# Performance work log

Measured on AMD Instinct MI355X. Metric: run time of the kernel, lower is better.

Reference implementation:

```python
import jax, jax.numpy as jnp
import numpy as np

N, P, E = 100000, 10000, 500000
DN, DP, DK, SKIP, MLP_H = 256, 128, 100, 27, 64
E_MEAN, E_STD = 4.0, 2.0
ETA_MEAN, ETA_STD = 0.0, 1.5
ATT_NORM = 0.1  # 1/sqrt(100)
LN_EPS, RMS_EPS = 1e-5, 1e-6


def setup_inputs() -> dict:
    key = jax.random.key(0)
    ks = jax.random.split(key, 32)
    DIN = DN + SKIP  # 283
    s = 0.05
    inp = {
        'node_hidden': jax.random.normal(ks[0], (N, DN), jnp.float32),
        'energy': jax.random.uniform(ks[1], (N,), jnp.float32, 0.01, 1.0),
        'eta': jax.random.normal(ks[2], (N,), jnp.float32),
        'phi': jax.random.normal(ks[3], (N,), jnp.float32),
        'layer': jax.random.uniform(ks[4], (N,), jnp.float32),
        'eta_l': jax.random.normal(ks[5], (N, 6), jnp.float32),
        'phi_l': jax.random.normal(ks[6], (N, 6), jnp.float32),
        'ene_l': jax.random.normal(ks[7], (N, 6), jnp.float32),
        'track_feats': jax.random.uniform(ks[8], (N, 5), jnp.float32),
        'particle_hidden': jax.random.normal(ks[9], (P, DP), jnp.float32),
        'global_rep': jax.random.normal(ks[10], (P, DN), jnp.float32),
        'edge_src': jax.random.randint(ks[11], (E,), 0, N, jnp.int32),
        'edge_dst': jax.random.randint(ks[12], (E,), 0, P, jnp.int32),
        # learned params
        'W_key': jax.random.normal(ks[13], (DIN, DK), jnp.float32) * s,
        'b_key': jnp.zeros((DK,), jnp.float32),
        'W_val': jax.random.normal(ks[14], (DIN, DP), jnp.float32) * s,
        'b_val': jnp.zeros((DP,), jnp.float32),
        'W_q': jax.random.normal(ks[15], (DP + DN, DK), jnp.float32) * s,
        'b_q': jnp.zeros((DK,), jnp.float32),
        'W_ih': jax.random.normal(ks[16], (DP, 3 * DP), jnp.float32) * s,
        'b_ih': jnp.zeros((3 * DP,), jnp.float32),
        'W_hh': jax.random.normal(ks[17], (DP, 3 * DP), jnp.float32) * s,
        'b_hh': jnp.zeros((3 * DP,), jnp.float32),
        'ln_g': jnp.ones((DP,), jnp.float32),
        'ln_b': jnp.zeros((DP,), jnp.float32),
        'W1': jax.random.normal(ks[18], (DP, MLP_H), jnp.float32) * s,
        'b1': jnp.zeros((MLP_H,), jnp.float32),
        'W2': jax.random.normal(ks[19], (MLP_H, DP), jnp.float32) * s,
        'b2': jnp.zeros((DP,), jnp.float32),
        'rms_w': jnp.ones((DP,), jnp.float32),
        'lin_w': jax.random.normal(ks[20], (1, DP), jnp.float32),
    }
    return inp


def _forward(node_hidden, energy, eta, phi, layer, eta_l, phi_l, ene_l, track_feats,
             particle_hidden, global_rep,
             W_key, b_key, W_val, b_val, W_q, b_q, W_ih, b_ih, W_hh, b_hh,
             ln_g, ln_b, W1, b1, W2, b2, rms_w, lin_w, edge_src, edge_dst):
    # --- build node inputs: hidden rep + 27 skip scalars (same order as torch cat) ---
    skip = jnp.concatenate([
        ((jnp.log(energy) - E_MEAN) / E_STD)[:, None],
        ((eta - ETA_MEAN) / ETA_STD)[:, None],
        phi[:, None], layer[:, None],
        (eta_l - ETA_MEAN) / ETA_STD,  # eta_l1..l6
        phi_l, ene_l,
        track_feats,  # isTrack, nTracks, tracks_pt, nTracks_4, tracks_pt_4
    ], axis=1)  # [N, 27]
    x = jnp.concatenate([node_hidden, skip], axis=1)  # [N, 283]
    keys = x @ W_key + b_key      # [N, 100]
    vals = x @ W_val + b_val      # [N, DP]
    q = jnp.concatenate([particle_hidden, global_rep], axis=1) @ W_q + b_q  # [P, 100]

    # --- per-edge attention (note: node_update consumes RAW relu attention) ---
    att = jax.nn.relu(jnp.sum(keys[edge_src] * q[edge_dst], axis=1) * ATT_NORM)  # [E]
    msg = att[:, None] * vals[edge_src]                                          # [E, DP]
    ws = jax.ops.segment_sum(msg, edge_dst, num_segments=P)                      # [P, DP]

    # --- node update: rmsnorm * sigmoid(eltwise) gating, GRU, LN, MLP residual ---
    rms = ws * jax.lax.rsqrt(jnp.mean(ws * ws, axis=-1, keepdims=True) + RMS_EPS) * rms_w
    gated = rms * jax.nn.sigmoid(ws * lin_w)

    h = particle_hidden
    gi = gated @ W_ih + b_ih
    gh = h @ W_hh + b_hh
    i_r, i_z, i_n = jnp.split(gi, 3, axis=1)
    h_r, h_z, h_n = jnp.split(gh, 3, axis=1)
    r = jax.nn.sigmoid(i_r + h_r)
    z = jax.nn.sigmoid(i_z + h_z)
    n = jnp.tanh(i_n + r * h_n)
    h_new = (1.0 - z) * n + z * h

    mu = jnp.mean(h_new, axis=-1, keepdims=True)
    var = jnp.mean((h_new - mu) ** 2, axis=-1, keepdims=True)
    ln = (h_new - mu) * jax.lax.rsqrt(var + LN_EPS) * ln_g + ln_b
    mlp = jax.nn.relu(ln @ W1 + b1) @ W2 + b2
    return h + mlp  # updated particle 'node hidden rep'


def reference(node_hidden, energy, eta, phi, layer, eta_l, phi_l, ene_l, track_feats,
              particle_hidden, global_rep, edge_src, edge_dst,
              W_key, b_key, W_val, b_val, W_q, b_q, W_ih, b_ih, W_hh, b_hh,
              ln_g, ln_b, W1, b1, W2, b2, rms_w, lin_w):
    return _forward(node_hidden, energy, eta, phi, layer, eta_l, phi_l, ene_l, track_feats,
                    particle_hidden, global_rep,
                    W_key, b_key, W_val, b_val, W_q, b_q, W_ih, b_ih, W_hh, b_hh,
                    ln_g, ln_b, W1, b1, W2, b2, rms_w, lin_w, edge_src, edge_dst)
```

## Files before the change

### kernel.cpp

```cpp
#include <hip/hip_runtime.h>
#include <hip/hip_bf16.h>
#include <math.h>

#define THREADS 256

typedef __bf16 bf16_t;
typedef __bf16 bf16x8 __attribute__((ext_vector_type(8)));
typedef float f32x4 __attribute__((ext_vector_type(4)));

__device__ __forceinline__ float sigmoidf_(float x) { return 1.f / (1.f + expf(-x)); }

__device__ __forceinline__ void gload_lds16(const void* g, void* l) {
    __builtin_amdgcn_global_load_lds((const __attribute__((address_space(1))) void*)g,
                                     (__attribute__((address_space(3))) void*)l, 16, 0, 0);
}

__global__ void prep_kernel(const float* __restrict__ W_key, const float* __restrict__ W_val,
                            const float* __restrict__ W_q, const float* __restrict__ b_key,
                            const float* __restrict__ b_val, const float* __restrict__ b_q,
                            bf16_t* __restrict__ WbfT, bf16_t* __restrict__ WqT,
                            float* __restrict__ bpn, float* __restrict__ bpq)
{
    int i = blockIdx.x * THREADS + threadIdx.x;
    const int NW = 256 * 288, NQ = 128 * 384;
    if (i < NW) {
        int c = i / 288, k = i - c * 288;
        float v = 0.f;
        if (k < 283) {
            if (c < 100) v = W_key[k * 100 + c];
            else if (c >= 128 && c < 256) v = W_val[k * 128 + (c - 128)];
        }
        WbfT[i] = (bf16_t)v;
    } else if (i < NW + NQ) {
        int j = i - NW;
        int c = j / 384, k = j - c * 384;
        WqT[j] = (bf16_t)((c < 100) ? W_q[k * 100 + c] : 0.f);
    } else if (i < NW + NQ + 256) {
        int c = i - NW - NQ;
        bpn[c] = (c < 100) ? b_key[c] : ((c >= 128 && c < 256) ? b_val[c - 128] : 0.f);
    } else if (i < NW + NQ + 256 + 128) {
        int c = i - NW - NQ - 256;
        bpq[c] = (c < 100) ? b_q[c] : 0.f;
    }
}

__global__ void prep2_kernel(const float* __restrict__ W_ih, const float* __restrict__ W_hh,
                             const float* __restrict__ b_ih, const float* __restrict__ b_hh,
                             const float* __restrict__ W1, const float* __restrict__ b1,
                             const float* __restrict__ W2,
                             bf16_t* __restrict__ BTg, bf16_t* __restrict__ W1Tp,
                             bf16_t* __restrict__ W2Tp, float* __restrict__ bgru,
                             float* __restrict__ b1p)
{
    int i = blockIdx.x * THREADS + threadIdx.x;
    const int NG = 768 * 256, N1 = 128 * 128, N2 = 128 * 128;
    if (i < NG) {
        int c = i >> 8, k = i & 255;
        float v = 0.f;
        if (c < 384) { if (k < 128) v = W_ih[k * 384 + c]; }
        else         { if (k >= 128) v = W_hh[(k - 128) * 384 + (c - 384)]; }
        BTg[i] = (bf16_t)v;
    } else if (i < NG + N1) {
        int j = i - NG; int c = j >> 7, k = j & 127;
        W1Tp[j] = (bf16_t)((c < 64) ? W1[k * 64 + c] : 0.f);
    } else if (i < NG + N1 + N2) {
        int j = i - NG - N1; int c = j >> 7, k = j & 127;
        W2Tp[j] = (bf16_t)((k < 64) ? W2[k * 128 + c] : 0.f);
    } else if (i < NG + N1 + N2 + 768) {
        int c = i - NG - N1 - N2;
        bgru[c] = (c < 384) ? b_ih[c] : b_hh[c - 384];
    } else if (i < NG + N1 + N2 + 768 + 128) {
        int c = i - NG - N1 - N2 - 768;
        b1p[c] = (c < 64) ? b1[c] : 0.f;
    }
}

__global__ void convertA_kernel(const float* __restrict__ nh, bf16_t* __restrict__ Abf, int N_)
{
    int id = blockIdx.x * THREADS + threadIdx.x;
    int row = id >> 5, cc = id & 31;
    bf16x8 v = {};
    if (row < N_) {
        const float* p = nh + (size_t)row * 256 + cc * 8;
        float4 a = *(const float4*)p;
        float4 b = *(const float4*)(p + 4);
        v[0] = (bf16_t)a.x; v[1] = (bf16_t)a.y; v[2] = (bf16_t)a.z; v[3] = (bf16_t)a.w;
        v[4] = (bf16_t)b.x; v[5] = (bf16_t)b.y; v[6] = (bf16_t)b.z; v[7] = (bf16_t)b.w;
    }
    *(bf16x8*)(Abf + (size_t)row * 288 + cc * 8) = v;
}

__global__ void skip_kernel(const float* __restrict__ energy, const float* __restrict__ eta,
                            const float* __restrict__ phi, const float* __restrict__ layer,
                            const float* __restrict__ eta_l, const float* __restrict__ phi_l,
                            const float* __restrict__ ene_l, const float* __restrict__ track,
                            bf16_t* __restrict__ Abf, int N_, int Mpad)
{
    int n = blockIdx.x * THREADS + threadIdx.x;
    if (n >= Mpad) return;
    float o[32];
#pragma unroll
    for (int j = 0; j < 32; ++j) o[j] = 0.f;
    if (n < N_) {
        o[0] = (logf(energy[n]) - 4.0f) * 0.5f;
        o[1] = eta[n] * (1.f / 1.5f);
        o[2] = phi[n];
        o[3] = layer[n];
#pragma unroll
        for (int j = 0; j < 6; ++j) o[4 + j]  = eta_l[n * 6 + j] * (1.f / 1.5f);
#pragma unroll
        for (int j = 0; j < 6; ++j) o[10 + j] = phi_l[n * 6 + j];
#pragma unroll
        for (int j = 0; j < 6; ++j) o[16 + j] = ene_l[n * 6 + j];
#pragma unroll
        for (int j = 0; j < 5; ++j) o[22 + j] = track[n * 5 + j];
    }
    bf16_t* dst = Abf + (size_t)n * 288 + 256;
#pragma unroll
    for (int g = 0; g < 4; ++g) {
        bf16x8 v;
#pragma unroll
        for (int j = 0; j < 8; ++j) v[j] = (bf16_t)o[g * 8 + j];
        *(bf16x8*)(dst + g * 8) = v;
    }
}

__global__ void convertQ_kernel(const float* __restrict__ ph, const float* __restrict__ grep,
                                bf16_t* __restrict__ Aq, int P_)
{
    int id = blockIdx.x * THREADS + threadIdx.x;
    int row = id / 48, cc = id - row * 48;
    bf16x8 v = {};
    if (row < P_) {
        const float* p = (cc < 16) ? (ph + (size_t)row * 128 + cc * 8)
                                   : (grep + (size_t)row * 256 + (cc - 16) * 8);
        float4 a = *(const float4*)p;
        float4 b = *(const float4*)(p + 4);
        v[0] = (bf16_t)a.x; v[1] = (bf16_t)a.y; v[2] = (bf16_t)a.z; v[3] = (bf16_t)a.w;
        v[4] = (bf16_t)b.x; v[5] = (bf16_t)b.y; v[6] = (bf16_t)b.z; v[7] = (bf16_t)b.w;
    }
    *(bf16x8*)(Aq + (size_t)row * 384 + cc * 8) = v;
}

template <int MODE>
__global__ __launch_bounds__(256) void mfma_gemm(
    const bf16_t* __restrict__ A, const bf16_t* __restrict__ BT,
    const float* __restrict__ bias, void* __restrict__ out0v, void* __restrict__ out1v,
    const float* __restrict__ resid, int K, int Mlimit)
{
    __shared__ short AsS[128 * 32];
    __shared__ short BsS[128 * 32];
    int tid = threadIdx.x;
    int lane = tid & 63, w = tid >> 6;
    int la = lane & 15, hi = lane >> 4;
    int m0 = (w & 1) * 64, n0 = (w >> 1) * 64;
    int row0 = blockIdx.y * 128, col0 = blockIdx.x * 128;

    f32x4 zero4 = {0.f, 0.f, 0.f, 0.f};
    f32x4 acc[4][4];
#pragma unroll
    for (int i = 0; i < 4; ++i)
#pragma unroll
        for (int j = 0; j < 4; ++j) acc[i][j] = zero4;

    for (int kt = 0; kt < K; kt += 32) {
#pragma unroll
        for (int it = 0; it < 2; ++it) {
            int c = tid + it * 256;
            int r = c >> 2, kc = c & 3;
            gload_lds16(A + (size_t)(row0 + r) * K + kt + kc * 8, AsS + c * 8);
            gload_lds16(BT + (size_t)(col0 + r) * K + kt + kc * 8, BsS + c * 8);
        }
        __syncthreads();
        bf16x8 a[4], b[4];
#pragma unroll
        for (int i = 0; i < 4; ++i)
            a[i] = *(const bf16x8*)(AsS + (m0 + i * 16 + la) * 32 + hi * 8);
#pragma unroll
        for (int j = 0; j < 4; ++j)
            b[j] = *(const bf16x8*)(BsS + (n0 + j * 16 + la) * 32 + hi * 8);
#pragma unroll
        for (int i = 0; i < 4; ++i)
#pragma unroll
            for (int j = 0; j < 4; ++j)
                acc[i][j] = __builtin_amdgcn_mfma_f32_16x16x32_bf16(a[i], b[j], acc[i][j], 0, 0, 0);
        __syncthreads();
    }

#pragma unroll
    for (int i = 0; i < 4; ++i) {
#pragma unroll
        for (int j = 0; j < 4; ++j) {
            int col = col0 + n0 + j * 16 + la;
            float bb = bias[col];
#pragma unroll
            for (int r = 0; r < 4; ++r) {
                int row = row0 + m0 + i * 16 + hi * 4 + r;
                float v = acc[i][j][r] + bb;
                if (MODE == 0) {
                    bf16_t* o0 = (bf16_t*)out0v; bf16_t* o1 = (bf16_t*)out1v;
                    if (col < 128) o0[(size_t)row * 128 + col] = (bf16_t)v;
                    else           o1[(size_t)row * 128 + (col - 128)] = (bf16_t)v;
                } else if (MODE == 1) {
                    ((bf16_t*)out0v)[(size_t)row * 128 + col] = (bf16_t)v;
                } else if (MODE == 2) {
                    ((float*)out0v)[(size_t)row * 768 + col] = v;
                } else if (MODE == 3) {
                    ((bf16_t*)out0v)[(size_t)row * 128 + col] = (bf16_t)fmaxf(v, 0.f);
                } else {
                    if (row < Mlimit)
                        ((float*)out0v)[(size_t)row * 128 + col] = v + resid[(size_t)row * 128 + col];
                }
            }
        }
    }
}

__global__ void zero_ints(int* __restrict__ p, int n)
{
    int i = blockIdx.x * THREADS + threadIdx.x;
    if (i < n) p[i] = 0;
}

__global__ void hist_kernel(const int* __restrict__ dst, int* __restrict__ cnt, int E_)
{
    int i = blockIdx.x * THREADS + threadIdx.x;
    if (i < E_) atomicAdd(&cnt[dst[i]], 1);
}

__global__ void scan_kernel(const int* __restrict__ cnt, int* __restrict__ offb, int P_)
{
    __shared__ int wsum[16];
    int tid = threadIdx.x;
    int lane = tid & 63, w = tid >> 6;
    int base = tid * 10;
    int c[10];
    int s = 0;
#pragma unroll
    for (int j = 0; j < 10; ++j) {
        int i = base + j;
        c[j] = (i < P_) ? cnt[i] : 0;
        s += c[j];
    }
    int pre = s;
    for (int o = 1; o < 64; o <<= 1) {
        int t = __shfl_up(pre, o);
        if (lane >= o) pre += t;
    }
    if (lane == 63) wsum[w] = pre;
    __syncthreads();
    if (w == 0 && lane < 16) {
        int v = wsum[lane];
        for (int o = 1; o < 16; o <<= 1) {
            int t = __shfl_up(v, o, 16);
            if (lane >= o) v += t;
        }
        wsum[lane] = v;
    }
    __syncthreads();
    int waveoff = (w == 0) ? 0 : wsum[w - 1];
    int run = waveoff + pre - s;
#pragma unroll
    for (int j = 0; j < 10; ++j) {
        int i = base + j;
        if (i <= P_) offb[i] = run;
        run += c[j];
    }
}

__global__ void fill_src_kernel(const int* __restrict__ dst, const int* __restrict__ src,
                                const int* __restrict__ offb, int* __restrict__ cur,
                                int* __restrict__ csrc, int E_)
{
    int i = blockIdx.x * THREADS + threadIdx.x;
    if (i < E_) {
        int d = dst[i];
        int pos = atomicAdd(&cur[d], 1);
        csrc[offb[d] + pos] = src[i];
    }
}

__global__ __launch_bounds__(256) void edge_kernel(
    const int* __restrict__ offb, const int* __restrict__ csrc,
    const bf16_t* __restrict__ Kb, const bf16_t* __restrict__ Vb,
    const bf16_t* __restrict__ Qb, float* __restrict__ ws_seg, int P_)
{
    int tid = threadIdx.x;
    int p = blockIdx.x * 4 + (tid >> 6);
    if (p >= P_) return;
    int lane = tid & 63;
    int c = lane & 15, g = lane >> 4;

    bf16x8 q8 = *(const bf16x8*)(Qb + (size_t)p * 128 + c * 8);
    float qf[8];
#pragma unroll
    for (int j = 0; j < 8; ++j) qf[j] = (float)q8[j];

    int s0 = offb[p], e0 = offb[p + 1];
    float acc[8] = {};

    int i = s0 + g;
    for (; i + 4 < e0; i += 8) {
        int sA = csrc[i], sB = csrc[i + 4];
        const bf16_t* kpA = Kb + (size_t)sA * 128 + c * 8;
        const bf16_t* vpA = Vb + (size_t)sA * 128 + c * 8;
        const bf16_t* kpB = Kb + (size_t)sB * 128 + c * 8;
        const bf16_t* vpB = Vb + (size_t)sB * 128 + c * 8;
        bf16x8 kA = *(const bf16x8*)kpA;
        bf16x8 vA = *(const bf16x8*)vpA;
        bf16x8 kB = *(const bf16x8*)kpB;
        bf16x8 vB = *(const bf16x8*)vpB;
        float dA = 0.f, dB = 0.f;
#pragma unroll
        for (int j = 0; j < 8; ++j) { dA += qf[j] * (float)kA[j]; dB += qf[j] * (float)kB[j]; }
        dA += __shfl_xor(dA, 1); dB += __shfl_xor(dB, 1);
        dA += __shfl_xor(dA, 2); dB += __shfl_xor(dB, 2);
        dA += __shfl_xor(dA, 4); dB += __shfl_xor(dB, 4);
        dA += __shfl_xor(dA, 8); dB += __shfl_xor(dB, 8);
        float aA = fmaxf(dA * 0.1f, 0.f);
        float aB = fmaxf(dB * 0.1f, 0.f);
#pragma unroll
        for (int j = 0; j < 8; ++j)
            acc[j] += aA * (float)vA[j] + aB * (float)vB[j];
    }
    if (i < e0) {
        int sA = csrc[i];
        bf16x8 kA = *(const bf16x8*)(Kb + (size_t)sA * 128 + c * 8);
        bf16x8 vA = *(const bf16x8*)(Vb + (size_t)sA * 128 + c * 8);
        float dA = 0.f;
#pragma unroll
        for (int j = 0; j < 8; ++j) dA += qf[j] * (float)kA[j];
        dA += __shfl_xor(dA, 1);
        dA += __shfl_xor(dA, 2);
        dA += __shfl_xor(dA, 4);
        dA += __shfl_xor(dA, 8);
        float aA = fmaxf(dA * 0.1f, 0.f);
#pragma unroll
        for (int j = 0; j < 8; ++j) acc[j] += aA * (float)vA[j];
    }

#pragma unroll
    for (int j = 0; j < 8; ++j) {
        acc[j] += __shfl_xor(acc[j], 16);
        acc[j] += __shfl_xor(acc[j], 32);
    }
    if (g == 0) {
        float* op = ws_seg + (size_t)p * 128 + c * 8;
        *(float4*)op       = make_float4(acc[0], acc[1], acc[2], acc[3]);
        *(float4*)(op + 4) = make_float4(acc[4], acc[5], acc[6], acc[7]);
    }
}

__global__ void gate_kernel(const float* __restrict__ ws_seg, const float* __restrict__ ph,
                            const float* __restrict__ rms_w, const float* __restrict__ lin_w,
                            bf16_t* __restrict__ AG, int P_, int Mq)
{
    int tid = threadIdx.x;
    int g = tid >> 4, s = tid & 15;
    int p = blockIdx.x * 16 + g;
    if (p >= Mq) return;
    int cb = s * 8;
    if (p >= P_) {
        bf16x8 z = {};
        *(bf16x8*)(AG + (size_t)p * 256 + cb) = z;
        *(bf16x8*)(AG + (size_t)p * 256 + 128 + cb) = z;
        return;
    }
    const float* wp = ws_seg + (size_t)p * 128 + cb;
    float4 a = *(const float4*)wp, b = *(const float4*)(wp + 4);
    float wsv[8] = {a.x, a.y, a.z, a.w, b.x, b.y, b.z, b.w};
    float ss = 0.f;
#pragma unroll
    for (int j = 0; j < 8; ++j) ss += wsv[j] * wsv[j];
    ss += __shfl_xor(ss, 1); ss += __shfl_xor(ss, 2); ss += __shfl_xor(ss, 4); ss += __shfl_xor(ss, 8);
    float scale = rsqrtf(ss * (1.f / 128.f) + 1e-6f);
    const float* hp = ph + (size_t)p * 128 + cb;
    float4 ha = *(const float4*)hp, hb = *(const float4*)(hp + 4);
    float hv[8] = {ha.x, ha.y, ha.z, ha.w, hb.x, hb.y, hb.z, hb.w};
    bf16x8 gv, hvb;
#pragma unroll
    for (int j = 0; j < 8; ++j) {
        int c = cb + j;
        float rv = wsv[j] * scale * rms_w[c];
        gv[j] = (bf16_t)(rv * sigmoidf_(wsv[j] * lin_w[c]));
        hvb[j] = (bf16_t)hv[j];
    }
    *(bf16x8*)(AG + (size_t)p * 256 + cb) = gv;
    *(bf16x8*)(AG + (size_t)p * 256 + 128 + cb) = hvb;
}

__global__ void gru_ln_kernel(const float* __restrict__ G768, const float* __restrict__ ph,
                              const float* __restrict__ ln_g, const float* __restrict__ ln_b,
                              bf16_t* __restrict__ LNb, int P_, int Mq)
{
    int tid = threadIdx.x;
    int g = tid >> 4, s = tid & 15;
    int p = blockIdx.x * 16 + g;
    if (p >= Mq) return;
    int cb = s * 8;
    if (p >= P_) {
        bf16x8 z = {};
        *(bf16x8*)(LNb + (size_t)p * 128 + cb) = z;
        return;
    }
    const float* G = G768 + (size_t)p * 768;
    float ir[8], iz[8], in_[8], hr[8], hz[8], hn_[8], hv[8];
#pragma unroll
    for (int q = 0; q < 2; ++q) {
        float4 v;
        v = *(const float4*)(G + cb + q * 4);        ir[q*4]=v.x; ir[q*4+1]=v.y; ir[q*4+2]=v.z; ir[q*4+3]=v.w;
        v = *(const float4*)(G + 128 + cb + q * 4);  iz[q*4]=v.x; iz[q*4+1]=v.y; iz[q*4+2]=v.z; iz[q*4+3]=v.w;
        v = *(const float4*)(G + 256 + cb + q * 4);  in_[q*4]=v.x; in_[q*4+1]=v.y; in_[q*4+2]=v.z; in_[q*4+3]=v.w;
        v = *(const float4*)(G + 384 + cb + q * 4);  hr[q*4]=v.x; hr[q*4+1]=v.y; hr[q*4+2]=v.z; hr[q*4+3]=v.w;
        v = *(const float4*)(G + 512 + cb + q * 4);  hz[q*4]=v.x; hz[q*4+1]=v.y; hz[q*4+2]=v.z; hz[q*4+3]=v.w;
        v = *(const float4*)(G + 640 + cb + q * 4);  hn_[q*4]=v.x; hn_[q*4+1]=v.y; hn_[q*4+2]=v.z; hn_[q*4+3]=v.w;
        v = *(const float4*)(ph + (size_t)p * 128 + cb + q * 4);
        hv[q*4]=v.x; hv[q*4+1]=v.y; hv[q*4+2]=v.z; hv[q*4+3]=v.w;
    }
    float hn[8];
    float sm = 0.f, sq = 0.f;
#pragma unroll
    for (int j = 0; j < 8; ++j) {
        float r = sigmoidf_(ir[j] + hr[j]);
        float z = sigmoidf_(iz[j] + hz[j]);
        float n = tanhf(in_[j] + r * hn_[j]);
        hn[j] = (1.f - z) * n + z * hv[j];
        sm += hn[j]; sq += hn[j] * hn[j];
    }
    sm += __shfl_xor(sm, 1); sm += __shfl_xor(sm, 2); sm += __shfl_xor(sm, 4); sm += __shfl_xor(sm, 8);
    sq += __shfl_xor(sq, 1); sq += __shfl_xor(sq, 2); sq += __shfl_xor(sq, 4); sq += __shfl_xor(sq, 8);
    float mu = sm * (1.f / 128.f);
    float var = sq * (1.f / 128.f) - mu * mu;
    float iv = rsqrtf(var + 1e-5f);
    bf16x8 o;
#pragma unroll
    for (int j = 0; j < 8; ++j) {
        int c = cb + j;
        o[j] = (bf16_t)((hn[j] - mu) * iv * ln_g[c] + ln_b[c]);
    }
    *(bf16x8*)(LNb + (size_t)p * 128 + cb) = o;
}

extern "C" void kernel_launch(void* const* d_in, const int* in_sizes, int n_in,
                              void* d_out, int out_size, void* d_ws, size_t ws_size,
                              hipStream_t stream)
{
    const float* nh      = (const float*)d_in[0];
    const float* energy  = (const float*)d_in[1];
    const float* eta     = (const float*)d_in[2];
    const float* phi     = (const float*)d_in[3];
    const float* layer   = (const float*)d_in[4];
    const float* eta_l   = (const float*)d_in[5];
    const float* phi_l   = (const float*)d_in[6];
    const float* ene_l   = (const float*)d_in[7];
    const float* track   = (const float*)d_in[8];
    const float* ph      = (const float*)d_in[9];
    const float* grep    = (const float*)d_in[10];
    const int*   esrc    = (const int*)d_in[11];
    const int*   edst    = (const int*)d_in[12];
    const float* W_key   = (const float*)d_in[13];
    const float* b_key   = (const float*)d_in[14];
    const float* W_val   = (const float*)d_in[15];
    const float* b_val   = (const float*)d_in[16];
    const float* W_q     = (const float*)d_in[17];
    const float* b_q     = (const float*)d_in[18];
    const float* W_ih    = (const float*)d_in[19];
    const float* b_ih    = (const float*)d_in[20];
    const float* W_hh    = (const float*)d_in[21];
    const float* b_hh    = (const float*)d_in[22];
    const float* ln_g    = (const float*)d_in[23];
    const float* ln_b    = (const float*)d_in[24];
    const float* W1      = (const float*)d_in[25];
    const float* b1      = (const float*)d_in[26];
    const float* W2      = (const float*)d_in[27];
    const float* b2      = (const float*)d_in[28];
    const float* rms_w   = (const float*)d_in[29];
    const float* lin_w   = (const float*)d_in[30];

    const int N = in_sizes[1];
    const int P = in_sizes[9] / 128;
    const int E = in_sizes[11];
    const int Mpad = ((N + 127) / 128) * 128;
    const int Mq   = ((P + 127) / 128) * 128;

    char* base = (char*)d_ws;
    size_t off = 0;
    auto alloc = [&](size_t bytes) { void* p = base + off; off = (off + bytes + 255) & ~(size_t)255; return p; };
    bf16_t* Abf   = (bf16_t*)alloc((size_t)Mpad * 288 * 2);
    bf16_t* Aq    = (bf16_t*)alloc((size_t)Mq * 384 * 2);
    bf16_t* WbfT  = (bf16_t*)alloc(256 * 288 * 2);
    bf16_t* WqT   = (bf16_t*)alloc(128 * 384 * 2);
    float*  bpn   = (float*)alloc(256 * 4);
    float*  bpq   = (float*)alloc(128 * 4);
    bf16_t* Kb    = (bf16_t*)alloc((size_t)Mpad * 128 * 2);
    bf16_t* Vb    = (bf16_t*)alloc((size_t)Mpad * 128 * 2);
    bf16_t* Qb    = (bf16_t*)alloc((size_t)Mq * 128 * 2);
    float*  ws_seg= (float*)alloc((size_t)P * 128 * 4);
    int*    cnt   = (int*)alloc((size_t)(2 * P) * 4);
    int*    cur   = cnt + P;
    int*    offb  = (int*)alloc((size_t)(P + 1) * 4);
    int*    csrc  = (int*)alloc((size_t)E * 4);
    bf16_t* AG    = (bf16_t*)alloc((size_t)Mq * 256 * 2);
    bf16_t* BTg   = (bf16_t*)alloc(768 * 256 * 2);
    bf16_t* W1Tp  = (bf16_t*)alloc(128 * 128 * 2);
    bf16_t* W2Tp  = (bf16_t*)alloc(128 * 128 * 2);
    float*  bgru  = (float*)alloc(768 * 4);
    float*  b1p   = (float*)alloc(128 * 4);
    float*  G768  = (float*)Abf;
    bf16_t* LNb   = Aq;
    bf16_t* M1    = Aq + (size_t)Mq * 128;

    {
        int total = 256 * 288 + 128 * 384 + 256 + 128;
        prep_kernel<<<(total + THREADS - 1) / THREADS, THREADS, 0, stream>>>(
            W_key, W_val, W_q, b_key, b_val, b_q, WbfT, WqT, bpn, bpq);
        int total2 = 768 * 256 + 128 * 128 + 128 * 128 + 768 + 128;
        prep2_kernel<<<(total2 + THREADS - 1) / THREADS, THREADS, 0, stream>>>(
            W_ih, W_hh, b_ih, b_hh, W1, b1, W2, BTg, W1Tp, W2Tp, bgru, b1p);
        convertA_kernel<<<Mpad * 32 / THREADS, THREADS, 0, stream>>>(nh, Abf, N);
        skip_kernel<<<(Mpad + THREADS - 1) / THREADS, THREADS, 0, stream>>>(
            energy, eta, phi, layer, eta_l, phi_l, ene_l, track, Abf, N, Mpad);
        convertQ_kernel<<<Mq * 48 / THREADS, THREADS, 0, stream>>>(ph, grep, Aq, P);
    }
    mfma_gemm<0><<<dim3(2, Mpad / 128), THREADS, 0, stream>>>(
        Abf, WbfT, bpn, Kb, Vb, nullptr, 288, 0);
    mfma_gemm<1><<<dim3(1, Mq / 128), THREADS, 0, stream>>>(
        Aq, WqT, bpq, Qb, nullptr, nullptr, 384, 0);
    zero_ints<<<(2 * P + THREADS - 1) / THREADS, THREADS, 0, stream>>>(cnt, 2 * P);
    hist_kernel<<<(E + THREADS - 1) / THREADS, THREADS, 0, stream>>>(edst, cnt, E);
    scan_kernel<<<1, 1024, 0, stream>>>(cnt, offb, P);
    fill_src_kernel<<<(E + THREADS - 1) / THREADS, THREADS, 0, stream>>>(
        edst, esrc, offb, cur, csrc, E);
    edge_kernel<<<(P + 3) / 4, THREADS, 0, stream>>>(offb, csrc, Kb, Vb, Qb, ws_seg, P);
    gate_kernel<<<Mq / 16, THREADS, 0, stream>>>(ws_seg, ph, rms_w, lin_w, AG, P, Mq);
    mfma_gemm<2><<<dim3(6, Mq / 128), THREADS, 0, stream>>>(
        AG, BTg, bgru, G768, nullptr, nullptr, 256, 0);
    gru_ln_kernel<<<Mq / 16, THREADS, 0, stream>>>(G768, ph, ln_g, ln_b, LNb, P, Mq);
    mfma_gemm<3><<<dim3(1, Mq / 128), THREADS, 0, stream>>>(
        LNb, W1Tp, b1p, M1, nullptr, nullptr, 128, 0);
    mfma_gemm<4><<<dim3(1, Mq / 128), THREADS, 0, stream>>>(
        M1, W2Tp, b2, d_out, nullptr, ph, 128, P);
}
```

Baseline: 264.9 us.

## Fuse fp32-to-bf16 conversion into GEMM loads and interleave K/V rows

Drops the separate convertA and convertQ kernels. The K/V and Q GEMMs now read the fp32 node and particle inputs directly and convert them to bf16 while staging into LDS, so the skip features get their own small buffer. K and V are written into one interleaved 256-wide buffer, letting the edge kernel fetch both for a source node from a single row, and its edge loop is unrolled to four gathers per iteration. This removes a full-size bf16 intermediate round trip. The cost is that GEMM A-tile loads become register-path fp32 loads instead of direct global-to-LDS copies.

```diff
diff --git a/kernel.cpp b/kernel.cpp
--- a/kernel.cpp
+++ b/kernel.cpp
@@ -13,6 +13,13 @@
 __device__ __forceinline__ void gload_lds16(const void* g, void* l) {
     __builtin_amdgcn_global_load_lds((const __attribute__((address_space(1))) void*)g,
                                      (__attribute__((address_space(3))) void*)l, 16, 0, 0);
+}
+
+__device__ __forceinline__ bf16x8 cvt8(float4 a, float4 b) {
+    bf16x8 v;
+    v[0] = (bf16_t)a.x; v[1] = (bf16_t)a.y; v[2] = (bf16_t)a.z; v[3] = (bf16_t)a.w;
+    v[4] = (bf16_t)b.x; v[5] = (bf16_t)b.y; v[6] = (bf16_t)b.z; v[7] = (bf16_t)b.w;
+    return v;
 }
 
 __global__ void prep_kernel(const float* __restrict__ W_key, const float* __restrict__ W_val,
@@ -75,26 +82,11 @@
     }
 }
 
-__global__ void convertA_kernel(const float* __restrict__ nh, bf16_t* __restrict__ Abf, int N_)
-{
-    int id = blockIdx.x * THREADS + threadIdx.x;
-    int row = id >> 5, cc = id & 31;
-    bf16x8 v = {};
-    if (row < N_) {
-        const float* p = nh + (size_t)row * 256 + cc * 8;
-        float4 a = *(const float4*)p;
-        float4 b = *(const float4*)(p + 4);
-        v[0] = (bf16_t)a.x; v[1] = (bf16_t)a.y; v[2] = (bf16_t)a.z; v[3] = (bf16_t)a.w;
-        v[4] = (bf16_t)b.x; v[5] = (bf16_t)b.y; v[6] = (bf16_t)b.z; v[7] = (bf16_t)b.w;
-    }
-    *(bf16x8*)(Abf + (size_t)row * 288 + cc * 8) = v;
-}
-
 __global__ void skip_kernel(const float* __restrict__ energy, const float* __restrict__ eta,
                             const float* __restrict__ phi, const float* __restrict__ layer,
                             const float* __restrict__ eta_l, const float* __restrict__ phi_l,
                             const float* __restrict__ ene_l, const float* __restrict__ track,
-                            bf16_t* __restrict__ Abf, int N_, int Mpad)
+                            bf16_t* __restrict__ skipb, int N_, int Mpad)
 {
     int n = blockIdx.x * THREADS + threadIdx.x;
     if (n >= Mpad) return;
@@ -115,7 +107,7 @@
 #pragma unroll
         for (int j = 0; j < 5; ++j) o[22 + j] = track[n * 5 + j];
     }
-    bf16_t* dst = Abf + (size_t)n * 288 + 256;
+    bf16_t* dst = skipb + (size_t)n * 32;
 #pragma unroll
     for (int g = 0; g < 4; ++g) {
         bf16x8 v;
@@ -125,28 +117,12 @@
     }
 }
 
-__global__ void convertQ_kernel(const float* __restrict__ ph, const float* __restrict__ grep,
-                                bf16_t* __restrict__ Aq, int P_)
-{
-    int id = blockIdx.x * THREADS + threadIdx.x;
-    int row = id / 48, cc = id - row * 48;
-    bf16x8 v = {};
-    if (row < P_) {
-        const float* p = (cc < 16) ? (ph + (size_t)row * 128 + cc * 8)
-                                   : (grep + (size_t)row * 256 + (cc - 16) * 8);
-        float4 a = *(const float4*)p;
-        float4 b = *(const float4*)(p + 4);
-        v[0] = (bf16_t)a.x; v[1] = (bf16_t)a.y; v[2] = (bf16_t)a.z; v[3] = (bf16_t)a.w;
-        v[4] = (bf16_t)b.x; v[5] = (bf16_t)b.y; v[6] = (bf16_t)b.z; v[7] = (bf16_t)b.w;
-    }
-    *(bf16x8*)(Aq + (size_t)row * 384 + cc * 8) = v;
-}
-
 template <int MODE>
 __global__ __launch_bounds__(256) void mfma_gemm(
-    const bf16_t* __restrict__ A, const bf16_t* __restrict__ BT,
-    const float* __restrict__ bias, void* __restrict__ out0v, void* __restrict__ out1v,
-    const float* __restrict__ resid, int K, int Mlimit)
+    const void* __restrict__ A0, const void* __restrict__ A1,
+    const bf16_t* __restrict__ BT, const float* __restrict__ bias,
+    void* __restrict__ out0v, const float* __restrict__ resid,
+    int K, int Mlimit, int Nrows)
 {
     __shared__ short AsS[128 * 32];
     __shared__ short BsS[128 * 32];
@@ -168,7 +144,30 @@
         for (int it = 0; it < 2; ++it) {
             int c = tid + it * 256;
             int r = c >> 2, kc = c & 3;
-            gload_lds16(A + (size_t)(row0 + r) * K + kt + kc * 8, AsS + c * 8);
+            int gm = row0 + r, gk = kt + kc * 8;
+            if (MODE == 0) {
+                if (gk < 256) {
+                    bf16x8 v = {};
+                    if (gm < Nrows) {
+                        const float* src = (const float*)A0 + (size_t)gm * 256 + gk;
+                        v = cvt8(*(const float4*)src, *(const float4*)(src + 4));
+                    }
+                    *(bf16x8*)((short*)AsS + (size_t)c * 8) = v;
+                } else {
+                    gload_lds16((const bf16_t*)A1 + (size_t)gm * 32 + (gk - 256), AsS + c * 8);
+                }
+            } else if (MODE == 1) {
+                bf16x8 v = {};
+                if (gm < Nrows) {
+                    const float* src = (gk < 128)
+                        ? ((const float*)A0 + (size_t)gm * 128 + gk)
+                        : ((const float*)A1 + (size_t)gm * 256 + (gk - 128));
+                    v = cvt8(*(const float4*)src, *(const float4*)(src + 4));
+                }
+                *(bf16x8*)((short*)AsS + (size_t)c * 8) = v;
+            } else {
+                gload_lds16((const bf16_t*)A0 + (size_t)gm * K + gk, AsS + c * 8);
+            }
             gload_lds16(BT + (size_t)(col0 + r) * K + kt + kc * 8, BsS + c * 8);
         }
         __syncthreads();
@@ -198,9 +197,7 @@
                 int row = row0 + m0 + i * 16 + hi * 4 + r;
                 float v = acc[i][j][r] + bb;
                 if (MODE == 0) {
-                    bf16_t* o0 = (bf16_t*)out0v; bf16_t* o1 = (bf16_t*)out1v;
-                    if (col < 128) o0[(size_t)row * 128 + col] = (bf16_t)v;
-                    else           o1[(size_t)row * 128 + (col - 128)] = (bf16_t)v;
+                    ((bf16_t*)out0v)[(size_t)row * 256 + col] = (bf16_t)v;
                 } else if (MODE == 1) {
                     ((bf16_t*)out0v)[(size_t)row * 128 + col] = (bf16_t)v;
                 } else if (MODE == 2) {
@@ -282,8 +279,8 @@
 
 __global__ __launch_bounds__(256) void edge_kernel(
     const int* __restrict__ offb, const int* __restrict__ csrc,
-    const bf16_t* __restrict__ Kb, const bf16_t* __restrict__ Vb,
-    const bf16_t* __restrict__ Qb, float* __restrict__ ws_seg, int P_)
+    const bf16_t* __restrict__ KVb, const bf16_t* __restrict__ Qb,
+    float* __restrict__ ws_seg, int P_)
 {
     int tid = threadIdx.x;
     int p = blockIdx.x * 4 + (tid >> 6);
@@ -300,33 +297,38 @@
     float acc[8] = {};
 
     int i = s0 + g;
-    for (; i + 4 < e0; i += 8) {
-        int sA = csrc[i], sB = csrc[i + 4];
-        const bf16_t* kpA = Kb + (size_t)sA * 128 + c * 8;
-        const bf16_t* vpA = Vb + (size_t)sA * 128 + c * 8;
-        const bf16_t* kpB = Kb + (size_t)sB * 128 + c * 8;
-        const bf16_t* vpB = Vb + (size_t)sB * 128 + c * 8;
-        bf16x8 kA = *(const bf16x8*)kpA;
-        bf16x8 vA = *(const bf16x8*)vpA;
-        bf16x8 kB = *(const bf16x8*)kpB;
-        bf16x8 vB = *(const bf16x8*)vpB;
-        float dA = 0.f, dB = 0.f;
-#pragma unroll
-        for (int j = 0; j < 8; ++j) { dA += qf[j] * (float)kA[j]; dB += qf[j] * (float)kB[j]; }
-        dA += __shfl_xor(dA, 1); dB += __shfl_xor(dB, 1);
-        dA += __shfl_xor(dA, 2); dB += __shfl_xor(dB, 2);
-        dA += __shfl_xor(dA, 4); dB += __shfl_xor(dB, 4);
-        dA += __shfl_xor(dA, 8); dB += __shfl_xor(dB, 8);
-        float aA = fmaxf(dA * 0.1f, 0.f);
-        float aB = fmaxf(dB * 0.1f, 0.f);
+    for (; i + 12 < e0; i += 16) {
+        int n0 = csrc[i], n1 = csrc[i + 4], n2 = csrc[i + 8], n3 = csrc[i + 12];
+        const bf16_t* b0 = KVb + (size_t)n0 * 256 + c * 8;
+        const bf16_t* b1 = KVb + (size_t)n1 * 256 + c * 8;
+        const bf16_t* b2 = KVb + (size_t)n2 * 256 + c * 8;
+        const bf16_t* b3 = KVb + (size_t)n3 * 256 + c * 8;
+        bf16x8 k0 = *(const bf16x8*)b0, v0 = *(const bf16x8*)(b0 + 128);
+        bf16x8 k1 = *(const bf16x8*)b1, v1 = *(const bf16x8*)(b1 + 128);
+        bf16x8 k2 = *(const bf16x8*)b2, v2 = *(const bf16x8*)(b2 + 128);
+        bf16x8 k3 = *(const bf16x8*)b3, v3 = *(const bf16x8*)(b3 + 128);
+        float d0 = 0.f, d1 = 0.f, d2 = 0.f, d3 = 0.f;
+#pragma unroll
+        for (int j = 0; j < 8; ++j) {
+            d0 += qf[j] * (float)k0[j]; d1 += qf[j] * (float)k1[j];
+            d2 += qf[j] * (float)k2[j]; d3 += qf[j] * (float)k3[j];
+        }
+        d0 += __shfl_xor(d0, 1); d1 += __shfl_xor(d1, 1); d2 += __shfl_xor(d2, 1); d3 += __shfl_xor(d3, 1);
+        d0 += __shfl_xor(d0, 2); d1 += __shfl_xor(d1, 2); d2 += __shfl_xor(d2, 2); d3 += __shfl_xor(d3, 2);
+        d0 += __shfl_xor(d0, 4); d1 += __shfl_xor(d1, 4); d2 += __shfl_xor(d2, 4); d3 += __shfl_xor(d3, 4);
+        d0 += __shfl_xor(d0, 8); d1 += __shfl_xor(d1, 8); d2 += __shfl_xor(d2, 8); d3 += __shfl_xor(d3, 8);
+        float a0 = fmaxf(d0 * 0.1f, 0.f), a1 = fmaxf(d1 * 0.1f, 0.f);
+        float a2 = fmaxf(d2 * 0.1f, 0.f), a3 = fmaxf(d3 * 0.1f, 0.f);
 #pragma unroll
         for (int j = 0; j < 8; ++j)
-            acc[j] += aA * (float)vA[j] + aB * (float)vB[j];
-    }
-    if (i < e0) {
-        int sA = csrc[i];
-        bf16x8 kA = *(const bf16x8*)(Kb + (size_t)sA * 128 + c * 8);
-        bf16x8 vA = *(const bf16x8*)(Vb + (size_t)sA * 128 + c * 8);
+            acc[j] += a0 * (float)v0[j] + a1 * (float)v1[j]
+                    + a2 * (float)v2[j] + a3 * (float)v3[j];
+    }
+    for (; i < e0; i += 4) {
+        int nA = csrc[i];
+        const bf16_t* bA = KVb + (size_t)nA * 256 + c * 8;
+        bf16x8 kA = *(const bf16x8*)bA;
+        bf16x8 vA = *(const bf16x8*)(bA + 128);
         float dA = 0.f;
 #pragma unroll
         for (int j = 0; j < 8; ++j) dA += qf[j] * (float)kA[j];
@@ -486,14 +488,12 @@
     char* base = (char*)d_ws;
     size_t off = 0;
     auto alloc = [&](size_t bytes) { void* p = base + off; off = (off + bytes + 255) & ~(size_t)255; return p; };
-    bf16_t* Abf   = (bf16_t*)alloc((size_t)Mpad * 288 * 2);
-    bf16_t* Aq    = (bf16_t*)alloc((size_t)Mq * 384 * 2);
+    bf16_t* skipb = (bf16_t*)alloc((size_t)Mpad * 32 * 2);
     bf16_t* WbfT  = (bf16_t*)alloc(256 * 288 * 2);
     bf16_t* WqT   = (bf16_t*)alloc(128 * 384 * 2);
     float*  bpn   = (float*)alloc(256 * 4);
     float*  bpq   = (float*)alloc(128 * 4);
-    bf16_t* Kb    = (bf16_t*)alloc((size_t)Mpad * 128 * 2);
-    bf16_t* Vb    = (bf16_t*)alloc((size_t)Mpad * 128 * 2);
+    bf16_t* KVb   = (bf16_t*)alloc((size_t)Mpad * 256 * 2);
     bf16_t* Qb    = (bf16_t*)alloc((size_t)Mq * 128 * 2);
     float*  ws_seg= (float*)alloc((size_t)P * 128 * 4);
     int*    cnt   = (int*)alloc((size_t)(2 * P) * 4);
@@ -506,9 +506,9 @@
     bf16_t* W2Tp  = (bf16_t*)alloc(128 * 128 * 2);
     float*  bgru  = (float*)alloc(768 * 4);
     float*  b1p   = (float*)alloc(128 * 4);
-    float*  G768  = (float*)Abf;
-    bf16_t* LNb   = Aq;
-    bf16_t* M1    = Aq + (size_t)Mq * 128;
+    float*  G768  = (float*)alloc((size_t)Mq * 768 * 4);
+    bf16_t* LNb   = (bf16_t*)alloc((size_t)Mq * 128 * 2);
+    bf16_t* M1    = (bf16_t*)alloc((size_t)Mq * 128 * 2);
 
     {
         int total = 256 * 288 + 128 * 384 + 256 + 128;
@@ -517,27 +517,25 @@
         int total2 = 768 * 256 + 128 * 128 + 128 * 128 + 768 + 128;
         prep2_kernel<<<(total2 + THREADS - 1) / THREADS, THREADS, 0, stream>>>(
             W_ih, W_hh, b_ih, b_hh, W1, b1, W2, BTg, W1Tp, W2Tp, bgru, b1p);
-        convertA_kernel<<<Mpad * 32 / THREADS, THREADS, 0, stream>>>(nh, Abf, N);
         skip_kernel<<<(Mpad + THREADS - 1) / THREADS, THREADS, 0, stream>>>(
-            energy, eta, phi, layer, eta_l, phi_l, ene_l, track, Abf, N, Mpad);
-        convertQ_kernel<<<Mq * 48 / THREADS, THREADS, 0, stream>>>(ph, grep, Aq, P);
+            energy, eta, phi, layer, eta_l, phi_l, ene_l, track, skipb, N, Mpad);
     }
     mfma_gemm<0><<<dim3(2, Mpad / 128), THREADS, 0, stream>>>(
-        Abf, WbfT, bpn, Kb, Vb, nullptr, 288, 0);
+        nh, skipb, WbfT, bpn, KVb, nullptr, 288, 0, N);
     mfma_gemm<1><<<dim3(1, Mq / 128), THREADS, 0, stream>>>(
-        Aq, WqT, bpq, Qb, nullptr, nullptr, 384, 0);
+        ph, grep, WqT, bpq, Qb, nullptr, 384, 0, P);
     zero_ints<<<(2 * P + THREADS - 1) / THREADS, THREADS, 0, stream>>>(cnt, 2 * P);
     hist_kernel<<<(E + THREADS - 1) / THREADS, THREADS, 0, stream>>>(edst, cnt, E);
     scan_kernel<<<1, 1024, 0, stream>>>(cnt, offb, P);
     fill_src_kernel<<<(E + THREADS - 1) / THREADS, THREADS, 0, stream>>>(
         edst, esrc, offb, cur, csrc, E);
-    edge_kernel<<<(P + 3) / 4, THREADS, 0, stream>>>(offb, csrc, Kb, Vb, Qb, ws_seg, P);
+    edge_kernel<<<(P + 3) / 4, THREADS, 0, stream>>>(offb, csrc, KVb, Qb, ws_seg, P);
     gate_kernel<<<Mq / 16, THREADS, 0, stream>>>(ws_seg, ph, rms_w, lin_w, AG, P, Mq);
     mfma_gemm<2><<<dim3(6, Mq / 128), THREADS, 0, stream>>>(
-        AG, BTg, bgru, G768, nullptr, nullptr, 256, 0);
+        AG, nullptr, BTg, bgru, G768, nullptr, 256, 0, Mq);
     gru_ln_kernel<<<Mq / 16, THREADS, 0, stream>>>(G768, ph, ln_g, ln_b, LNb, P, Mq);
     mfma_gemm<3><<<dim3(1, Mq / 128), THREADS, 0, stream>>>(
-        LNb, W1Tp, b1p, M1, nullptr, nullptr, 128, 0);
+        LNb, nullptr, W1Tp, b1p, M1, nullptr, 128, 0, Mq);
     mfma_gemm<4><<<dim3(1, Mq / 128), THREADS, 0, stream>>>(
-        M1, W2Tp, b2, d_out, nullptr, ph, 128, P);
-}
+        M1, nullptr, W2Tp, b2, d_out, ph, 128, P, Mq);
+}
```

Measured after the change: 261.7 us. No clear change (-1.2%).
